# Kernel optimization log

Hardware: AMD Instinct MI355X
Metric: run time of the kernel (lower is better)

Reference implementation:

```python
import jax, jax.numpy as jnp
import numpy as np

N_NODES = 25000
N_EDGES = 400000
D_FEAT = 64      # 2 * per-endpoint feature dim (concat of both endpoints)
STATE_DIM = 16
OUT_DIM = 16
MAX_IT = 5
THRESHOLD = 0.01


def setup_inputs() -> dict:
    key = jax.random.key(0)
    ks = jax.random.split(key, 8)
    edge_src = jax.random.randint(ks[0], (N_EDGES,), 0, N_NODES)
    edge_dst = jax.random.randint(ks[1], (N_EDGES,), 0, N_NODES)
    edge_feat = jax.random.normal(ks[2], (N_EDGES, D_FEAT), jnp.float32)
    w = lambda k, s: jax.random.normal(k, s, jnp.float32) * 0.1
    return {
        "edge_feat": edge_feat,
        "Wst1": w(ks[3], (D_FEAT + STATE_DIM, 2 * STATE_DIM)),
        "bst1": jnp.zeros((2 * STATE_DIM,), jnp.float32),
        "Wst2": w(ks[4], (2 * STATE_DIM, STATE_DIM)),
        "bst2": jnp.zeros((STATE_DIM,), jnp.float32),
        "Wout1": w(ks[5], (STATE_DIM, 2 * STATE_DIM)),
        "bout1": jnp.zeros((2 * STATE_DIM,), jnp.float32),
        "Wout2": w(ks[6], (2 * STATE_DIM, OUT_DIM)),
        "bout2": jnp.zeros((OUT_DIM,), jnp.float32),
        "edge_src": edge_src,
        "edge_dst": edge_dst,
        "n_nodes": N_NODES,
    }


def reference(edge_feat, Wst1, bst1, Wst2, bst2, Wout1, bout1, Wout2, bout2,
              edge_src, edge_dst, n_nodes):
    s = Wst2.shape[1]
    state0 = jnp.zeros((n_nodes, s), edge_feat.dtype)

    def step(carry, _):
        state, done = carry
        gat = state[edge_dst]                                   # [E, s] gather
        x = jnp.concatenate([edge_feat, gat], axis=1)           # [E, 2d+s]
        res = jnp.tanh(jnp.tanh(x @ Wst1 + bst1) @ Wst2 + bst2)  # state MLP
        new_state = jax.ops.segment_sum(res, edge_src, num_segments=n_nodes)
        # per-node L2 change; stop (freeze) once all nodes are below threshold
        dist = jnp.sqrt(jnp.sum((new_state - state) ** 2, axis=1) + 1e-10)
        converged = jnp.all(dist <= THRESHOLD)
        state = jnp.where(done, state, new_state)
        return (state, done | converged), None

    (state, _), _ = jax.lax.scan(step, (state0, jnp.array(False)), None, length=MAX_IT)
    h = jnp.tanh(state @ Wout1 + bout1)
    out = jax.nn.softmax(h @ Wout2 + bout2, axis=-1)  # [n_nodes, out_dim]
    return out
```

## Files before the change

### kernel.cpp

```cpp
#include <hip/hip_runtime.h>
#include <cstddef>

#define D_FEAT 64
#define S_DIM 16
#define H_DIM 32
#define OUT_DIM 16
#define MAX_IT 5

typedef _Float16 half8 __attribute__((ext_vector_type(8)));

__device__ __forceinline__ float fast_tanh(float x) {
    float xc = fminf(fmaxf(x, -15.0f), 15.0f);
    float e = __expf(2.0f * xc);
    return (e - 1.0f) / (e + 1.0f);
}

__global__ __launch_bounds__(256)
void k_hist(const int* __restrict__ src, int* __restrict__ deg, int E) {
    int e = blockIdx.x * 256 + threadIdx.x;
    if (e < E) atomicAdd(&deg[src[e]], 1);
}

__global__ __launch_bounds__(1024)
void k_scan(const int* __restrict__ deg, int* __restrict__ cursor, int N) {
    __shared__ int wsum[16];
    __shared__ int carry;
    int lane = threadIdx.x & 63;
    int wid = threadIdx.x >> 6;
    if (threadIdx.x == 0) carry = 0;
    __syncthreads();
    for (int base = 0; base < N; base += 1024) {
        int i = base + (int)threadIdx.x;
        int v = (i < N) ? deg[i] : 0;
        int incl = v;
#pragma unroll
        for (int off = 1; off < 64; off <<= 1) {
            int t = __shfl_up(incl, off, 64);
            if (lane >= off) incl += t;
        }
        if (lane == 63) wsum[wid] = incl;
        __syncthreads();
        if (wid == 0) {
            int w = (lane < 16) ? wsum[lane] : 0;
            int wi = w;
#pragma unroll
            for (int off = 1; off < 16; off <<= 1) {
                int t = __shfl_up(wi, off, 64);
                if (lane >= off) wi += t;
            }
            if (lane < 16) wsum[lane] = wi - w;
        }
        __syncthreads();
        int excl = incl - v + wsum[wid] + carry;
        if (i < N) cursor[i] = excl;
        __syncthreads();
        if ((int)threadIdx.x == 1023) carry = excl + v;
        __syncthreads();
    }
}

__global__ __launch_bounds__(256)
void k_scatter(const int* __restrict__ src, const int* __restrict__ dst,
               int* __restrict__ cursor, int* __restrict__ pos,
               int* __restrict__ dstp, int* __restrict__ srcp, int E) {
    int e = blockIdx.x * 256 + threadIdx.x;
    if (e >= E) return;
    int s = src[e];
    int p = atomicAdd(&cursor[s], 1);
    pos[e] = p;
    dstp[p] = dst[e];
    srcp[p] = s;
}

__global__ __launch_bounds__(256)
void k_pre(const float* __restrict__ feat, const float* __restrict__ Wst1,
           const float* __restrict__ bst1, const int* __restrict__ pos,
           _Float16* __restrict__ pre, int E) {
    int e = blockIdx.x * 256 + threadIdx.x;
    if (e >= E) return;
    float acc[H_DIM];
#pragma unroll
    for (int j = 0; j < H_DIM; ++j) acc[j] = bst1[j];
    const float4* f4 = reinterpret_cast<const float4*>(feat + (size_t)e * D_FEAT);
#pragma unroll 4
    for (int k4 = 0; k4 < D_FEAT / 4; ++k4) {
        float4 v = f4[k4];
        const float* w = Wst1 + k4 * 4 * H_DIM;
#pragma unroll
        for (int j = 0; j < H_DIM; ++j) acc[j] = fmaf(v.x, w[j], acc[j]);
#pragma unroll
        for (int j = 0; j < H_DIM; ++j) acc[j] = fmaf(v.y, w[H_DIM + j], acc[j]);
#pragma unroll
        for (int j = 0; j < H_DIM; ++j) acc[j] = fmaf(v.z, w[2 * H_DIM + j], acc[j]);
#pragma unroll
        for (int j = 0; j < H_DIM; ++j) acc[j] = fmaf(v.w, w[3 * H_DIM + j], acc[j]);
    }
    int p = pos[e];
    half8* op = reinterpret_cast<half8*>(pre + (size_t)p * H_DIM);
#pragma unroll
    for (int j8 = 0; j8 < 4; ++j8) {
        half8 v;
#pragma unroll
        for (int k = 0; k < 8; ++k) v[k] = (_Float16)acc[j8 * 8 + k];
        op[j8] = v;
    }
}

__global__ __launch_bounds__(256)
void k_edge(const _Float16* __restrict__ pre, const float* __restrict__ nodeH,
            const int* __restrict__ dstp, const int* __restrict__ srcp,
            const float* __restrict__ Wst2, const float* __restrict__ bst2,
            float* __restrict__ new_state, const int* __restrict__ flags, int E) {
    if (flags[0]) return;
    __shared__ float sres[256][20];
    __shared__ int ssrc[256];
    int base = blockIdx.x * 256;
    int t = threadIdx.x;
    int ep = base + t;
    int s = (ep < E) ? srcp[ep] : (int)0x80000000;
    ssrc[t] = s;
    float res[S_DIM];
    if (ep < E) {
        int d = dstp[ep];
        const half8* pp = reinterpret_cast<const half8*>(pre + (size_t)ep * H_DIM);
        const float4* hp = reinterpret_cast<const float4*>(nodeH + (size_t)d * H_DIM);
        float h[H_DIM];
#pragma unroll
        for (int j8 = 0; j8 < 4; ++j8) {
            half8 pv = pp[j8];
            float4 a = hp[j8 * 2], b = hp[j8 * 2 + 1];
            h[j8 * 8 + 0] = fast_tanh((float)pv[0] + a.x);
            h[j8 * 8 + 1] = fast_tanh((float)pv[1] + a.y);
            h[j8 * 8 + 2] = fast_tanh((float)pv[2] + a.z);
            h[j8 * 8 + 3] = fast_tanh((float)pv[3] + a.w);
            h[j8 * 8 + 4] = fast_tanh((float)pv[4] + b.x);
            h[j8 * 8 + 5] = fast_tanh((float)pv[5] + b.y);
            h[j8 * 8 + 6] = fast_tanh((float)pv[6] + b.z);
            h[j8 * 8 + 7] = fast_tanh((float)pv[7] + b.w);
        }
        float r[S_DIM];
#pragma unroll
        for (int i = 0; i < S_DIM; ++i) r[i] = bst2[i];
#pragma unroll
        for (int j = 0; j < H_DIM; ++j) {
            const float* w = Wst2 + (size_t)j * S_DIM;
            float hj = h[j];
#pragma unroll
            for (int i = 0; i < S_DIM; ++i) r[i] = fmaf(hj, w[i], r[i]);
        }
#pragma unroll
        for (int i = 0; i < S_DIM; ++i) {
            res[i] = fast_tanh(r[i]);
            sres[t][i] = res[i];
        }
    }
    __syncthreads();
    if (ep >= E) return;
    bool local_head = (t == 0) || (ssrc[t - 1] != s);
    if (!local_head) return;
    float acc[S_DIM];
#pragma unroll
    for (int i = 0; i < S_DIM; ++i) acc[i] = res[i];
    int t2 = t + 1;
    while (t2 < 256 && base + t2 < E && ssrc[t2] == s) {
#pragma unroll
        for (int i = 0; i < S_DIM; ++i) acc[i] += sres[t2][i];
        ++t2;
    }
    bool trueStart = (t > 0) || (ep == 0) || (srcp[ep - 1] != s);
    int ge = base + t2;
    bool trueEnd = (t2 < 256) || (ge >= E) || (srcp[ge] != s);
    float* ns = new_state + (size_t)s * S_DIM;
    if (trueStart && trueEnd) {
        float4* nsp = reinterpret_cast<float4*>(ns);
        nsp[0] = make_float4(acc[0], acc[1], acc[2], acc[3]);
        nsp[1] = make_float4(acc[4], acc[5], acc[6], acc[7]);
        nsp[2] = make_float4(acc[8], acc[9], acc[10], acc[11]);
        nsp[3] = make_float4(acc[12], acc[13], acc[14], acc[15]);
    } else {
#pragma unroll
        for (int i = 0; i < S_DIM; ++i) atomicAdd(ns + i, acc[i]);
    }
}

__global__ __launch_bounds__(256)
void k_node(float* __restrict__ state, float* __restrict__ new_state,
            float* __restrict__ nodeH, const float* __restrict__ Wst1,
            int* __restrict__ flags, int N) {
    if (flags[0]) return;
    int tt = blockIdx.x * 256 + threadIdx.x;
    int n = tt >> 2;
    int q = tt & 3;
    if (n >= N) return;
    float4* nsp = reinterpret_cast<float4*>(new_state + (size_t)n * S_DIM);
    float4* sp = reinterpret_cast<float4*>(state + (size_t)n * S_DIM);
    float4 acc = nsp[q];
    float4 old = sp[q];
    float dx = acc.x - old.x, dy = acc.y - old.y, dz = acc.z - old.z, dw = acc.w - old.w;
    float d2 = dx * dx + dy * dy + dz * dz + dw * dw;
    sp[q] = acc;
    nsp[q] = make_float4(0.f, 0.f, 0.f, 0.f);
    d2 += __shfl_xor(d2, 1);
    d2 += __shfl_xor(d2, 2);
    if (q == 0 && d2 + 1e-10f > 1e-4f) flags[1] = 1;

    float st[S_DIM];
    st[q * 4 + 0] = acc.x; st[q * 4 + 1] = acc.y; st[q * 4 + 2] = acc.z; st[q * 4 + 3] = acc.w;
#pragma unroll
    for (int m = 1; m < 4; ++m) {
        int qs = q ^ m;
        st[qs * 4 + 0] = __shfl_xor(acc.x, m);
        st[qs * 4 + 1] = __shfl_xor(acc.y, m);
        st[qs * 4 + 2] = __shfl_xor(acc.z, m);
        st[qs * 4 + 3] = __shfl_xor(acc.w, m);
    }
    float hh[8];
#pragma unroll
    for (int j = 0; j < 8; ++j) hh[j] = 0.f;
#pragma unroll
    for (int k = 0; k < S_DIM; ++k) {
        const float* w = Wst1 + (size_t)(D_FEAT + k) * H_DIM + q * 8;
        float sk = st[k];
#pragma unroll
        for (int j = 0; j < 8; ++j) hh[j] = fmaf(sk, w[j], hh[j]);
    }
    float4* hp = reinterpret_cast<float4*>(nodeH + (size_t)n * H_DIM + q * 8);
    hp[0] = make_float4(hh[0], hh[1], hh[2], hh[3]);
    hp[1] = make_float4(hh[4], hh[5], hh[6], hh[7]);
}

__global__ void gnn_flag(int* flags) {
    if (flags[1] == 0) flags[0] = 1;
    flags[1] = 0;
}

__global__ __launch_bounds__(256)
void gnn_out(const float* __restrict__ state, const float* __restrict__ Wout1,
             const float* __restrict__ bout1, const float* __restrict__ Wout2,
             const float* __restrict__ bout2, float* __restrict__ out, int N) {
    int n = blockIdx.x * 256 + threadIdx.x;
    if (n >= N) return;
    float st[S_DIM];
    const float4* sp = reinterpret_cast<const float4*>(state + (size_t)n * S_DIM);
    float4 v0 = sp[0], v1 = sp[1], v2 = sp[2], v3 = sp[3];
    st[0] = v0.x; st[1] = v0.y; st[2] = v0.z; st[3] = v0.w;
    st[4] = v1.x; st[5] = v1.y; st[6] = v1.z; st[7] = v1.w;
    st[8] = v2.x; st[9] = v2.y; st[10] = v2.z; st[11] = v2.w;
    st[12] = v3.x; st[13] = v3.y; st[14] = v3.z; st[15] = v3.w;

    float h[H_DIM];
#pragma unroll
    for (int j = 0; j < H_DIM; ++j) {
        float acc = bout1[j];
#pragma unroll
        for (int k = 0; k < S_DIM; ++k) acc = fmaf(st[k], Wout1[(size_t)k * H_DIM + j], acc);
        h[j] = fast_tanh(acc);
    }
    float l[OUT_DIM];
#pragma unroll
    for (int i = 0; i < OUT_DIM; ++i) l[i] = bout2[i];
#pragma unroll
    for (int j = 0; j < H_DIM; ++j) {
        float hj = h[j];
#pragma unroll
        for (int i = 0; i < OUT_DIM; ++i) l[i] = fmaf(hj, Wout2[(size_t)j * OUT_DIM + i], l[i]);
    }
    float m = l[0];
#pragma unroll
    for (int i = 1; i < OUT_DIM; ++i) m = fmaxf(m, l[i]);
    float sum = 0.0f;
#pragma unroll
    for (int i = 0; i < OUT_DIM; ++i) {
        float tv = __expf(l[i] - m);
        l[i] = tv;
        sum += tv;
    }
    float inv = 1.0f / sum;
    float4* op = reinterpret_cast<float4*>(out + (size_t)n * OUT_DIM);
    op[0] = make_float4(l[0] * inv, l[1] * inv, l[2] * inv, l[3] * inv);
    op[1] = make_float4(l[4] * inv, l[5] * inv, l[6] * inv, l[7] * inv);
    op[2] = make_float4(l[8] * inv, l[9] * inv, l[10] * inv, l[11] * inv);
    op[3] = make_float4(l[12] * inv, l[13] * inv, l[14] * inv, l[15] * inv);
}

extern "C" void kernel_launch(void* const* d_in, const int* in_sizes, int n_in,
                              void* d_out, int out_size, void* d_ws, size_t ws_size,
                              hipStream_t stream) {
    const float* edge_feat = (const float*)d_in[0];
    const float* Wst1 = (const float*)d_in[1];
    const float* bst1 = (const float*)d_in[2];
    const float* Wst2 = (const float*)d_in[3];
    const float* bst2 = (const float*)d_in[4];
    const float* Wout1 = (const float*)d_in[5];
    const float* bout1 = (const float*)d_in[6];
    const float* Wout2 = (const float*)d_in[7];
    const float* bout2 = (const float*)d_in[8];
    const int* esrc = (const int*)d_in[9];
    const int* edst = (const int*)d_in[10];
    const int E = in_sizes[9];
    const int N = out_size / OUT_DIM;
    float* out = (float*)d_out;

    float* state = (float*)d_ws;
    float* nodeH = state + (size_t)N * S_DIM;
    float* new_state = nodeH + (size_t)N * H_DIM;
    _Float16* pre = (_Float16*)(new_state + (size_t)N * S_DIM);
    int* pos = (int*)(pre + (size_t)E * H_DIM);
    int* dstp = pos + E;
    int* srcp = dstp + E;
    int* deg = srcp + E;
    int* cursor = deg + N;
    int* flags = cursor + N;

    hipMemsetAsync(state, 0, (size_t)N * (S_DIM + H_DIM + S_DIM) * sizeof(float), stream);
    hipMemsetAsync(deg, 0, (size_t)N * sizeof(int), stream);
    hipMemsetAsync(flags, 0, 2 * sizeof(int), stream);

    int ebl = (E + 255) / 256;
    int nbl = (N + 255) / 256;
    int rbl = (N * 4 + 255) / 256;

    k_hist<<<ebl, 256, 0, stream>>>(esrc, deg, E);
    k_scan<<<1, 1024, 0, stream>>>(deg, cursor, N);
    k_scatter<<<ebl, 256, 0, stream>>>(esrc, edst, cursor, pos, dstp, srcp, E);
    k_pre<<<ebl, 256, 0, stream>>>(edge_feat, Wst1, bst1, pos, pre, E);

    for (int it = 0; it < MAX_IT; ++it) {
        k_edge<<<ebl, 256, 0, stream>>>(pre, nodeH, dstp, srcp, Wst2, bst2,
                                        new_state, flags, E);
        k_node<<<rbl, 256, 0, stream>>>(state, new_state, nodeH, Wst1, flags, N);
        gnn_flag<<<1, 1, 0, stream>>>(flags);
    }
    gnn_out<<<nbl, 256, 0, stream>>>(state, Wout1, bout1, Wout2, bout2, out, N);
}
```

Measured before the change: 333.5 us.

## Stage edge features and pre-activations through LDS, replace flag kernel with per-iteration flags

k_pre now loads edge features cooperatively into shared memory with a rotated (swizzled) layout, so global reads are coalesced instead of each thread striding over its own row. k_edge stages the fp16 pre-activation block through shared memory the same way and reads segment partial sums as float4. The single-thread gnn_flag kernel is removed: each iteration writes its own flag slot, and later kernels check all earlier slots to decide whether to exit. This drops five kernel launches but adds a syncthreads plus extra shared memory per block, which may lower occupancy.

```diff
diff --git a/kernel.cpp b/kernel.cpp
--- a/kernel.cpp
+++ b/kernel.cpp
@@ -76,32 +76,52 @@
 void k_pre(const float* __restrict__ feat, const float* __restrict__ Wst1,
            const float* __restrict__ bst1, const int* __restrict__ pos,
            _Float16* __restrict__ pre, int E) {
-    int e = blockIdx.x * 256 + threadIdx.x;
-    if (e >= E) return;
+    __shared__ float sfeat[256 * 32];
+    const int t = threadIdx.x;
+    const int base = blockIdx.x * 256;
+    const int e = base + t;
+    const bool valid = e < E;
     float acc[H_DIM];
 #pragma unroll
     for (int j = 0; j < H_DIM; ++j) acc[j] = bst1[j];
-    const float4* f4 = reinterpret_cast<const float4*>(feat + (size_t)e * D_FEAT);
-#pragma unroll 4
-    for (int k4 = 0; k4 < D_FEAT / 4; ++k4) {
-        float4 v = f4[k4];
-        const float* w = Wst1 + k4 * 4 * H_DIM;
-#pragma unroll
-        for (int j = 0; j < H_DIM; ++j) acc[j] = fmaf(v.x, w[j], acc[j]);
-#pragma unroll
-        for (int j = 0; j < H_DIM; ++j) acc[j] = fmaf(v.y, w[H_DIM + j], acc[j]);
-#pragma unroll
-        for (int j = 0; j < H_DIM; ++j) acc[j] = fmaf(v.z, w[2 * H_DIM + j], acc[j]);
-#pragma unroll
-        for (int j = 0; j < H_DIM; ++j) acc[j] = fmaf(v.w, w[3 * H_DIM + j], acc[j]);
-    }
-    int p = pos[e];
-    half8* op = reinterpret_cast<half8*>(pre + (size_t)p * H_DIM);
+
+#pragma unroll
+    for (int p = 0; p < 2; ++p) {
+#pragma unroll
+        for (int i = 0; i < 8; ++i) {
+            int idx4 = t + i * 256;
+            int r = idx4 >> 3;
+            int c0 = (idx4 & 7) * 4;
+            if (base + r < E) {
+                const float4 v = *reinterpret_cast<const float4*>(
+                    feat + (size_t)(base + r) * D_FEAT + p * 32 + c0);
+                sfeat[r * 32 + ((c0 + 0 + r) & 31)] = v.x;
+                sfeat[r * 32 + ((c0 + 1 + r) & 31)] = v.y;
+                sfeat[r * 32 + ((c0 + 2 + r) & 31)] = v.z;
+                sfeat[r * 32 + ((c0 + 3 + r) & 31)] = v.w;
+            }
+        }
+        __syncthreads();
+        if (valid) {
+            const float* wbase = Wst1 + (size_t)p * 32 * H_DIM;
+#pragma unroll
+            for (int k = 0; k < 32; ++k) {
+                float v = sfeat[t * 32 + ((k + t) & 31)];
+                const float* w = wbase + k * H_DIM;
+#pragma unroll
+                for (int j = 0; j < H_DIM; ++j) acc[j] = fmaf(v, w[j], acc[j]);
+            }
+        }
+        __syncthreads();
+    }
+    if (!valid) return;
+    int p16 = pos[e];
+    half8* op = reinterpret_cast<half8*>(pre + (size_t)p16 * H_DIM);
 #pragma unroll
     for (int j8 = 0; j8 < 4; ++j8) {
         half8 v;
 #pragma unroll
-        for (int k = 0; k < 8; ++k) v[k] = (_Float16)acc[j8 * 8 + k];
+        for (int kk = 0; kk < 8; ++kk) v[kk] = (_Float16)acc[j8 * 8 + kk];
         op[j8] = v;
     }
 }
@@ -110,33 +130,53 @@
 void k_edge(const _Float16* __restrict__ pre, const float* __restrict__ nodeH,
             const int* __restrict__ dstp, const int* __restrict__ srcp,
             const float* __restrict__ Wst2, const float* __restrict__ bst2,
-            float* __restrict__ new_state, const int* __restrict__ flags, int E) {
-    if (flags[0]) return;
+            float* __restrict__ new_state, const int* __restrict__ flags,
+            int it, int E) {
+#pragma unroll
+    for (int j = 0; j < MAX_IT; ++j)
+        if (j < it && flags[2 + j] == 0) return;
+    __shared__ float spre[256 * 16];
     __shared__ float sres[256][20];
     __shared__ int ssrc[256];
-    int base = blockIdx.x * 256;
-    int t = threadIdx.x;
-    int ep = base + t;
-    int s = (ep < E) ? srcp[ep] : (int)0x80000000;
+    const int t = threadIdx.x;
+    const int base = blockIdx.x * 256;
+    const int ep = base + t;
+    const bool valid = ep < E;
+
+    const int navail4 = (E - base) * 4;
+    const float4* psrc = reinterpret_cast<const float4*>(pre + (size_t)base * H_DIM);
+#pragma unroll
+    for (int i = 0; i < 4; ++i) {
+        int idx4 = t + i * 256;
+        if (idx4 < navail4) {
+            float4 v = psrc[idx4];
+            int r = idx4 >> 2;
+            int c0 = (idx4 & 3) * 4;
+            spre[r * 16 + ((c0 + 0 + r) & 15)] = v.x;
+            spre[r * 16 + ((c0 + 1 + r) & 15)] = v.y;
+            spre[r * 16 + ((c0 + 2 + r) & 15)] = v.z;
+            spre[r * 16 + ((c0 + 3 + r) & 15)] = v.w;
+        }
+    }
+    int s = valid ? srcp[ep] : (int)0x80000000;
     ssrc[t] = s;
+    int d = valid ? dstp[ep] : 0;
+    __syncthreads();
+
     float res[S_DIM];
-    if (ep < E) {
-        int d = dstp[ep];
-        const half8* pp = reinterpret_cast<const half8*>(pre + (size_t)ep * H_DIM);
+    if (valid) {
         const float4* hp = reinterpret_cast<const float4*>(nodeH + (size_t)d * H_DIM);
         float h[H_DIM];
 #pragma unroll
-        for (int j8 = 0; j8 < 4; ++j8) {
-            half8 pv = pp[j8];
-            float4 a = hp[j8 * 2], b = hp[j8 * 2 + 1];
-            h[j8 * 8 + 0] = fast_tanh((float)pv[0] + a.x);
-            h[j8 * 8 + 1] = fast_tanh((float)pv[1] + a.y);
-            h[j8 * 8 + 2] = fast_tanh((float)pv[2] + a.z);
-            h[j8 * 8 + 3] = fast_tanh((float)pv[3] + a.w);
-            h[j8 * 8 + 4] = fast_tanh((float)pv[4] + b.x);
-            h[j8 * 8 + 5] = fast_tanh((float)pv[5] + b.y);
-            h[j8 * 8 + 6] = fast_tanh((float)pv[6] + b.z);
-            h[j8 * 8 + 7] = fast_tanh((float)pv[7] + b.w);
+        for (int q = 0; q < 8; ++q) {
+            float4 a = hp[q];
+            union { float f; _Float16 hh[2]; } c0v, c1v;
+            c0v.f = spre[t * 16 + ((2 * q + 0 + t) & 15)];
+            c1v.f = spre[t * 16 + ((2 * q + 1 + t) & 15)];
+            h[4 * q + 0] = fast_tanh((float)c0v.hh[0] + a.x);
+            h[4 * q + 1] = fast_tanh((float)c0v.hh[1] + a.y);
+            h[4 * q + 2] = fast_tanh((float)c1v.hh[0] + a.z);
+            h[4 * q + 3] = fast_tanh((float)c1v.hh[1] + a.w);
         }
         float r[S_DIM];
 #pragma unroll
@@ -155,7 +195,7 @@
         }
     }
     __syncthreads();
-    if (ep >= E) return;
+    if (!valid) return;
     bool local_head = (t == 0) || (ssrc[t - 1] != s);
     if (!local_head) return;
     float acc[S_DIM];
@@ -163,8 +203,12 @@
     for (int i = 0; i < S_DIM; ++i) acc[i] = res[i];
     int t2 = t + 1;
     while (t2 < 256 && base + t2 < E && ssrc[t2] == s) {
-#pragma unroll
-        for (int i = 0; i < S_DIM; ++i) acc[i] += sres[t2][i];
+        const float4* rp = reinterpret_cast<const float4*>(&sres[t2][0]);
+        float4 a0 = rp[0], a1 = rp[1], a2 = rp[2], a3 = rp[3];
+        acc[0] += a0.x; acc[1] += a0.y; acc[2] += a0.z; acc[3] += a0.w;
+        acc[4] += a1.x; acc[5] += a1.y; acc[6] += a1.z; acc[7] += a1.w;
+        acc[8] += a2.x; acc[9] += a2.y; acc[10] += a2.z; acc[11] += a2.w;
+        acc[12] += a3.x; acc[13] += a3.y; acc[14] += a3.z; acc[15] += a3.w;
         ++t2;
     }
     bool trueStart = (t > 0) || (ep == 0) || (srcp[ep - 1] != s);
@@ -186,8 +230,10 @@
 __global__ __launch_bounds__(256)
 void k_node(float* __restrict__ state, float* __restrict__ new_state,
             float* __restrict__ nodeH, const float* __restrict__ Wst1,
-            int* __restrict__ flags, int N) {
-    if (flags[0]) return;
+            int* __restrict__ flags, int it, int N) {
+#pragma unroll
+    for (int j = 0; j < MAX_IT; ++j)
+        if (j < it && flags[2 + j] == 0) return;
     int tt = blockIdx.x * 256 + threadIdx.x;
     int n = tt >> 2;
     int q = tt & 3;
@@ -202,7 +248,7 @@
     nsp[q] = make_float4(0.f, 0.f, 0.f, 0.f);
     d2 += __shfl_xor(d2, 1);
     d2 += __shfl_xor(d2, 2);
-    if (q == 0 && d2 + 1e-10f > 1e-4f) flags[1] = 1;
+    if (q == 0 && d2 + 1e-10f > 1e-4f) flags[2 + it] = 1;
 
     float st[S_DIM];
     st[q * 4 + 0] = acc.x; st[q * 4 + 1] = acc.y; st[q * 4 + 2] = acc.z; st[q * 4 + 3] = acc.w;
@@ -227,11 +273,6 @@
     float4* hp = reinterpret_cast<float4*>(nodeH + (size_t)n * H_DIM + q * 8);
     hp[0] = make_float4(hh[0], hh[1], hh[2], hh[3]);
     hp[1] = make_float4(hh[4], hh[5], hh[6], hh[7]);
-}
-
-__global__ void gnn_flag(int* flags) {
-    if (flags[1] == 0) flags[0] = 1;
-    flags[1] = 0;
 }
 
 __global__ __launch_bounds__(256)
@@ -314,7 +355,7 @@
 
     hipMemsetAsync(state, 0, (size_t)N * (S_DIM + H_DIM + S_DIM) * sizeof(float), stream);
     hipMemsetAsync(deg, 0, (size_t)N * sizeof(int), stream);
-    hipMemsetAsync(flags, 0, 2 * sizeof(int), stream);
+    hipMemsetAsync(flags, 0, 8 * sizeof(int), stream);
 
     int ebl = (E + 255) / 256;
     int nbl = (N + 255) / 256;
@@ -327,9 +368,8 @@
 
     for (int it = 0; it < MAX_IT; ++it) {
         k_edge<<<ebl, 256, 0, stream>>>(pre, nodeH, dstp, srcp, Wst2, bst2,
-                                        new_state, flags, E);
-        k_node<<<rbl, 256, 0, stream>>>(state, new_state, nodeH, Wst1, flags, N);
-        gnn_flag<<<1, 1, 0, stream>>>(flags);
+                                        new_state, flags, it, E);
+        k_node<<<rbl, 256, 0, stream>>>(state, new_state, nodeH, Wst1, flags, it, N);
     }
     gnn_out<<<nbl, 256, 0, stream>>>(state, Wout1, bout1, Wout2, bout2, out, N);
 }
```

After: 365.0 us. 9.5% more time.

## Parallelize segmented reduction across segment-dims and drop per-iteration flag kernel

Applied to the files above, without the earlier changes.

The edge kernel's segment reduction changes from one thread per segment head, which loops serially over the run, to a layout where every (segment, dim) pair is handled by its own thread. Segment ends are found with a wave shuffle-min scan, and segment heads are compacted into shared memory. The single-thread gnn_flag kernel is removed, and each iteration now writes its own convergence flag slot, which later kernels check directly. This spreads the reduction more evenly across threads and saves 5 tiny launches, but adds extra syncthreads, shared-memory traffic and more atomics per dim.

```diff
diff --git a/kernel.cpp b/kernel.cpp
--- a/kernel.cpp
+++ b/kernel.cpp
@@ -110,17 +110,29 @@
 void k_edge(const _Float16* __restrict__ pre, const float* __restrict__ nodeH,
             const int* __restrict__ dstp, const int* __restrict__ srcp,
             const float* __restrict__ Wst2, const float* __restrict__ bst2,
-            float* __restrict__ new_state, const int* __restrict__ flags, int E) {
-    if (flags[0]) return;
-    __shared__ float sres[256][20];
+            float* __restrict__ new_state, const int* __restrict__ flags,
+            int it, int E) {
+#pragma unroll
+    for (int j = 0; j < MAX_IT; ++j)
+        if (j < it && flags[2 + j] == 0) return;
+    __shared__ float sres[256][17];
     __shared__ int ssrc[256];
-    int base = blockIdx.x * 256;
-    int t = threadIdx.x;
-    int ep = base + t;
-    int s = (ep < E) ? srcp[ep] : (int)0x80000000;
+    __shared__ int send[256];
+    __shared__ int segs[256];
+    __shared__ int wf[4];
+    __shared__ int nseg;
+    const int t = threadIdx.x;
+    const int lane = t & 63;
+    const int wid = t >> 6;
+    const int base = blockIdx.x * 256;
+    const int ep = base + t;
+    const bool valid = ep < E;
+    if (t == 0) nseg = 0;
+
+    int s = valid ? srcp[ep] : (int)0x80000000;
     ssrc[t] = s;
-    float res[S_DIM];
-    if (ep < E) {
+
+    if (valid) {
         int d = dstp[ep];
         const half8* pp = reinterpret_cast<const half8*>(pre + (size_t)ep * H_DIM);
         const float4* hp = reinterpret_cast<const float4*>(nodeH + (size_t)d * H_DIM);
@@ -149,45 +161,55 @@
             for (int i = 0; i < S_DIM; ++i) r[i] = fmaf(hj, w[i], r[i]);
         }
 #pragma unroll
-        for (int i = 0; i < S_DIM; ++i) {
-            res[i] = fast_tanh(r[i]);
-            sres[t][i] = res[i];
-        }
+        for (int i = 0; i < S_DIM; ++i) sres[t][i] = fast_tanh(r[i]);
     }
     __syncthreads();
-    if (ep >= E) return;
-    bool local_head = (t == 0) || (ssrc[t - 1] != s);
-    if (!local_head) return;
-    float acc[S_DIM];
-#pragma unroll
-    for (int i = 0; i < S_DIM; ++i) acc[i] = res[i];
-    int t2 = t + 1;
-    while (t2 < 256 && base + t2 < E && ssrc[t2] == s) {
-#pragma unroll
-        for (int i = 0; i < S_DIM; ++i) acc[i] += sres[t2][i];
-        ++t2;
-    }
-    bool trueStart = (t > 0) || (ep == 0) || (srcp[ep - 1] != s);
-    int ge = base + t2;
-    bool trueEnd = (t2 < 256) || (ge >= E) || (srcp[ge] != s);
-    float* ns = new_state + (size_t)s * S_DIM;
-    if (trueStart && trueEnd) {
-        float4* nsp = reinterpret_cast<float4*>(ns);
-        nsp[0] = make_float4(acc[0], acc[1], acc[2], acc[3]);
-        nsp[1] = make_float4(acc[4], acc[5], acc[6], acc[7]);
-        nsp[2] = make_float4(acc[8], acc[9], acc[10], acc[11]);
-        nsp[3] = make_float4(acc[12], acc[13], acc[14], acc[15]);
-    } else {
-#pragma unroll
-        for (int i = 0; i < S_DIM; ++i) atomicAdd(ns + i, acc[i]);
+
+    bool head = (t == 0) || (ssrc[t - 1] != s);
+    bool tail = (t == 255) || (ssrc[t + 1] != s);
+
+    int mn = tail ? (t + 1) : 0x7fffffff;
+#pragma unroll
+    for (int off = 1; off < 64; off <<= 1) {
+        int u = __shfl_down(mn, off, 64);
+        if (lane + off < 64) mn = min(mn, u);
+    }
+    if (lane == 0) wf[wid] = mn;
+    __syncthreads();
+    int carry = 0x7fffffff;
+#pragma unroll
+    for (int w = 0; w < 4; ++w)
+        if (w > wid) carry = min(carry, wf[w]);
+    send[t] = min(mn, carry);
+    int spos = -1;
+    if (head && valid) spos = atomicAdd(&nseg, 1);
+    if (spos >= 0) segs[spos] = t;
+    __syncthreads();
+
+    int ns = nseg;
+    for (int w = t; w < ns * 16; w += 256) {
+        int st = segs[w >> 4];
+        int dim = w & 15;
+        int en = send[st];
+        int node = ssrc[st];
+        float a = 0.f;
+        for (int i = st; i < en; ++i) a += sres[i][dim];
+        bool tS = (st > 0) || (base == 0) || (srcp[base - 1] != node);
+        int gen = base + en;
+        bool tE = (en < 256) || (gen >= E) || (srcp[gen] != node);
+        float* p = new_state + (size_t)node * S_DIM + dim;
+        if (tS && tE) *p = a;
+        else atomicAdd(p, a);
     }
 }
 
 __global__ __launch_bounds__(256)
 void k_node(float* __restrict__ state, float* __restrict__ new_state,
             float* __restrict__ nodeH, const float* __restrict__ Wst1,
-            int* __restrict__ flags, int N) {
-    if (flags[0]) return;
+            int* __restrict__ flags, int it, int N) {
+#pragma unroll
+    for (int j = 0; j < MAX_IT; ++j)
+        if (j < it && flags[2 + j] == 0) return;
     int tt = blockIdx.x * 256 + threadIdx.x;
     int n = tt >> 2;
     int q = tt & 3;
@@ -202,7 +224,7 @@
     nsp[q] = make_float4(0.f, 0.f, 0.f, 0.f);
     d2 += __shfl_xor(d2, 1);
     d2 += __shfl_xor(d2, 2);
-    if (q == 0 && d2 + 1e-10f > 1e-4f) flags[1] = 1;
+    if (q == 0 && d2 + 1e-10f > 1e-4f) flags[2 + it] = 1;
 
     float st[S_DIM];
     st[q * 4 + 0] = acc.x; st[q * 4 + 1] = acc.y; st[q * 4 + 2] = acc.z; st[q * 4 + 3] = acc.w;
@@ -227,11 +249,6 @@
     float4* hp = reinterpret_cast<float4*>(nodeH + (size_t)n * H_DIM + q * 8);
     hp[0] = make_float4(hh[0], hh[1], hh[2], hh[3]);
     hp[1] = make_float4(hh[4], hh[5], hh[6], hh[7]);
-}
-
-__global__ void gnn_flag(int* flags) {
-    if (flags[1] == 0) flags[0] = 1;
-    flags[1] = 0;
 }
 
 __global__ __launch_bounds__(256)
@@ -314,7 +331,7 @@
 
     hipMemsetAsync(state, 0, (size_t)N * (S_DIM + H_DIM + S_DIM) * sizeof(float), stream);
     hipMemsetAsync(deg, 0, (size_t)N * sizeof(int), stream);
-    hipMemsetAsync(flags, 0, 2 * sizeof(int), stream);
+    hipMemsetAsync(flags, 0, 8 * sizeof(int), stream);
 
     int ebl = (E + 255) / 256;
     int nbl = (N + 255) / 256;
@@ -327,9 +344,8 @@
 
     for (int it = 0; it < MAX_IT; ++it) {
         k_edge<<<ebl, 256, 0, stream>>>(pre, nodeH, dstp, srcp, Wst2, bst2,
-                                        new_state, flags, E);
-        k_node<<<rbl, 256, 0, stream>>>(state, new_state, nodeH, Wst1, flags, N);
-        gnn_flag<<<1, 1, 0, stream>>>(flags);
+                                        new_state, flags, it, E);
+        k_node<<<rbl, 256, 0, stream>>>(state, new_state, nodeH, Wst1, flags, it, N);
     }
     gnn_out<<<nbl, 256, 0, stream>>>(state, Wout1, bout1, Wout2, bout2, out, N);
 }
```

After: 304.1 us. -8.8%, faster.
